# Kernel tuning notes

Hardware: AMD Instinct MI355X
Metric: run time of the kernel (lower is better)

Reference implementation:

```python
import jax, jax.numpy as jnp
import numpy as np

B, S, D, H = 2, 2048, 1024, 16
DK = D // H  # 64


def setup_inputs() -> dict:
    key = jax.random.key(0)
    k0, k1, k2, k3, k4, k5, k6 = jax.random.split(key, 7)
    scale = 0.02
    return {
        "q": jax.random.normal(k0, (B, S, D), dtype=jnp.float32),
        "k": jax.random.normal(k1, (B, S, D), dtype=jnp.float32),
        "v": jax.random.normal(k2, (B, S, D), dtype=jnp.float32),
        # per-head Q/K projection weights (n_head separate Linear layers, bias=False)
        "Wq": jax.random.normal(k3, (H, D, DK), dtype=jnp.float32) * scale,
        "Wk": jax.random.normal(k4, (H, D, DK), dtype=jnp.float32) * scale,
        # shared V projection (the same v_layer object is reused for every head)
        "Wv": jax.random.normal(k5, (D, DK), dtype=jnp.float32) * scale,
        # output projection fc: d_v -> d_model, bias=False
        "Wo": jax.random.normal(k6, (DK, D), dtype=jnp.float32) * scale,
    }


def reference(q, k, v, Wq, Wk, Wv, Wo):
    d_k = Wq.shape[-1]
    # batched per-head projections (replaces the Python loop over heads)
    qs = jnp.einsum("bsd,hdk->bhsk", q, Wq)          # [B,H,S,DK]
    ks = jnp.einsum("bsd,hdk->bhsk", k, Wk)          # [B,H,S,DK]
    vs = jnp.einsum("bsd,dk->bsk", v, Wv)            # [B,S,DK] shared across heads
    scores = jnp.einsum("bhsk,bhtk->bhst", qs, ks) / jnp.sqrt(
        jnp.asarray(d_k, dtype=jnp.float32)
    )                                                 # [B,H,S,S]
    attn = jax.nn.softmax(scores, axis=-1)            # [B,H,S,S]; dropout = identity (eval)
    heads = jnp.einsum("bhst,btk->bhsk", attn, vs)    # [B,H,S,DK]
    head = heads.mean(axis=1)                         # mean over heads, not concat
    attn_mean = attn.mean(axis=1)                     # [B,S,S]
    out = jnp.einsum("bsk,kd->bsd", head, Wo)         # [B,S,D]; dropout = identity
    return (out, attn_mean)
```

## Files before the change

### kernel.cpp

```cpp
#include <hip/hip_runtime.h>

#define B_ 2
#define S_ 2048
#define D_ 1024
#define H_ 16
#define DK_ 64

typedef __bf16 bf8 __attribute__((ext_vector_type(8)));
typedef float f4 __attribute__((ext_vector_type(4)));
typedef unsigned short u16x8 __attribute__((ext_vector_type(8)));

__device__ __forceinline__ unsigned short f2bf_bits(float f) {
  unsigned int u = __float_as_uint(f);
  return (unsigned short)((u + 0x7fffu + ((u >> 16) & 1u)) >> 16);
}

__device__ __forceinline__ bf8 pack_bf8(f4 lo, f4 hi) {
  u16x8 u;
  u[0] = f2bf_bits(lo[0]); u[1] = f2bf_bits(lo[1]);
  u[2] = f2bf_bits(lo[2]); u[3] = f2bf_bits(lo[3]);
  u[4] = f2bf_bits(hi[0]); u[5] = f2bf_bits(hi[1]);
  u[6] = f2bf_bits(hi[2]); u[7] = f2bf_bits(hi[3]);
  union { u16x8 u; bf8 b; } x; x.u = u; return x.b;
}

__device__ __forceinline__ bf8 ldb(const unsigned short* p) {
  return *reinterpret_cast<const bf8*>(p);
}

__device__ __forceinline__ void stage16(const void* g, void* l) {
  __builtin_amdgcn_global_load_lds(
      (const __attribute__((address_space(1))) void*)g,
      (__attribute__((address_space(3))) void*)l, 16, 0, 0);
}

#define MFMA(a, b, c) __builtin_amdgcn_mfma_f32_16x16x32_bf16((a), (b), (c), 0, 0, 0)

__global__ void k_prep(const float* __restrict__ q, const float* __restrict__ k,
                       const float* __restrict__ wq, const float* __restrict__ wk,
                       const float* __restrict__ wv, const float* __restrict__ wo,
                       unsigned short* __restrict__ qb, unsigned short* __restrict__ kb,
                       unsigned short* __restrict__ wqt, unsigned short* __restrict__ wkt,
                       unsigned short* __restrict__ wvt, unsigned short* __restrict__ wot) {
  __shared__ float tl[64 * 65];
  int bid = blockIdx.x, tid = threadIdx.x;
  const int rr = tid >> 6, cc = tid & 63;
  if (bid < 4096) {
    int which = bid >> 11;
    long i = ((long)(bid & 2047) * 256 + tid) * 8;
    const float* src = which ? k : q;
    unsigned short* dst = which ? kb : qb;
    f4 lo = *reinterpret_cast<const f4*>(src + i);
    f4 hi = *reinterpret_cast<const f4*>(src + i + 4);
    *reinterpret_cast<bf8*>(dst + i) = pack_bf8(lo, hi);
  } else if (bid < 4352) {
    int blk = bid - 4096;
    int h = blk >> 4, d0 = (blk & 15) * 64;
    for (int m = 0; m < 2; ++m) {
      const float* src = m ? wk : wq;
      unsigned short* dst = m ? wkt : wqt;
      if (m) __syncthreads();
#pragma unroll
      for (int it = 0; it < 16; ++it) {
        int d = it * 4 + rr;
        tl[cc * 65 + d] = src[(long)h * 65536 + (d0 + d) * 64 + cc];
      }
      __syncthreads();
#pragma unroll
      for (int it = 0; it < 16; ++it) {
        int n = it * 4 + rr;
        dst[(long)h * 65536 + n * 1024 + d0 + cc] = f2bf_bits(tl[n * 65 + cc]);
      }
    }
  } else if (bid < 4368) {
    int d0 = (bid - 4352) * 64;
#pragma unroll
    for (int it = 0; it < 16; ++it) {
      int d = it * 4 + rr;
      tl[cc * 65 + d] = wv[(long)(d0 + d) * 64 + cc];
    }
    __syncthreads();
#pragma unroll
    for (int it = 0; it < 16; ++it) {
      int n = it * 4 + rr;
      wvt[(long)n * 1024 + d0 + cc] = f2bf_bits(tl[n * 65 + cc]);
    }
  } else {
    int d0 = (bid - 4368) * 64;
#pragma unroll
    for (int it = 0; it < 16; ++it) {
      int kk = it * 4 + rr;
      tl[cc * 65 + kk] = wo[(long)kk * 1024 + d0 + cc];
    }
    __syncthreads();
#pragma unroll
    for (int it = 0; it < 16; ++it) {
      int ddl = it * 4 + rr;
      wot[(long)(d0 + ddl) * 64 + cc] = f2bf_bits(tl[ddl * 65 + cc]);
    }
  }
}

__global__ __launch_bounds__(256) void k_gemm_qk(
    const unsigned short* __restrict__ qb, const unsigned short* __restrict__ kb,
    const unsigned short* __restrict__ wqt, const unsigned short* __restrict__ wkt,
    unsigned short* __restrict__ qsb, unsigned short* __restrict__ ksb) {
  __shared__ unsigned short lds[8192];
  const int tid = threadIdx.x, wave = tid >> 6, lane = tid & 63;
  const int l15 = lane & 15, quad = lane >> 4;
  const int m0 = blockIdx.x * 128, n0 = blockIdx.y * 128;
  const int which = blockIdx.z;
  const unsigned short* A = which ? kb : qb;
  const unsigned short* W = which ? wkt : wqt;
  unsigned short* C = which ? ksb : qsb;
  const float scale = which ? 1.0f : 0.18033688011112042f;
  const int wr = wave >> 1, wc = wave & 1;

  f4 acc[4][4];
#pragma unroll
  for (int i = 0; i < 4; ++i)
#pragma unroll
    for (int j = 0; j < 4; ++j) acc[i][j] = f4{0.f, 0.f, 0.f, 0.f};

  const int sl15 = tid & 15, squad = (tid >> 4) & 3, st = tid >> 6;
  const unsigned short* gA = A + (long)(m0 + st * 16 + sl15) * D_ + squad * 8;
  const unsigned short* gB = W + (long)(n0 + st * 16 + sl15) * D_ + squad * 8;

  for (int k0 = 0; k0 < D_; k0 += 32) {
    stage16(gA + k0, lds + tid * 8);
    stage16(gA + 64 * D_ + k0, lds + 2048 + tid * 8);
    stage16(gB + k0, lds + 4096 + tid * 8);
    stage16(gB + 64 * D_ + k0, lds + 6144 + tid * 8);
    __syncthreads();
    bf8 aF[4], bF[4];
#pragma unroll
    for (int mi = 0; mi < 4; ++mi)
      aF[mi] = ldb(lds + (wr * 4 + mi) * 512 + lane * 8);
#pragma unroll
    for (int ni = 0; ni < 4; ++ni)
      bF[ni] = ldb(lds + 4096 + (wc * 4 + ni) * 512 + lane * 8);
#pragma unroll
    for (int mi = 0; mi < 4; ++mi)
#pragma unroll
      for (int ni = 0; ni < 4; ++ni)
        acc[mi][ni] = MFMA(aF[mi], bF[ni], acc[mi][ni]);
    __syncthreads();
  }
#pragma unroll
  for (int mi = 0; mi < 4; ++mi)
#pragma unroll
    for (int r = 0; r < 4; ++r) {
      long row = m0 + wr * 64 + mi * 16 + quad * 4 + r;
#pragma unroll
      for (int ni = 0; ni < 4; ++ni)
        C[row * D_ + n0 + wc * 64 + ni * 16 + l15] = f2bf_bits(acc[mi][ni][r] * scale);
    }
}

__global__ __launch_bounds__(256) void k_pv(
    const float* __restrict__ v, const unsigned short* __restrict__ wvt,
    float* __restrict__ pv) {
  const int tid = threadIdx.x, wave = tid >> 6, lane = tid & 63;
  const int l15 = lane & 15, quad = lane >> 4;
  const int rg = blockIdx.x, kc = blockIdx.y;
  const int row0 = rg * 64 + wave * 16;
  const float* arow = v + (long)(row0 + l15) * D_ + kc * 256 + quad * 8;
  const unsigned short* wbase = wvt + kc * 256 + quad * 8;
  f4 acc[4];
  for (int i = 0; i < 4; ++i) acc[i] = f4{0.f, 0.f, 0.f, 0.f};
  for (int k0 = 0; k0 < 256; k0 += 32) {
    f4 alo = *reinterpret_cast<const f4*>(arow + k0);
    f4 ahi = *reinterpret_cast<const f4*>(arow + k0 + 4);
    bf8 a = pack_bf8(alo, ahi);
#pragma unroll
    for (int i = 0; i < 4; ++i) {
      bf8 bf = ldb(wbase + (long)(i * 16 + l15) * D_ + k0);
      acc[i] = MFMA(a, bf, acc[i]);
    }
  }
#pragma unroll
  for (int i = 0; i < 4; ++i)
#pragma unroll
    for (int r = 0; r < 4; ++r)
      pv[((long)kc * 4096 + row0 + quad * 4 + r) * 64 + i * 16 + l15] = acc[i][r];
}

__global__ void k_vred(const float* __restrict__ pv, unsigned short* __restrict__ vst) {
  int e = blockIdx.x * 256 + threadIdx.x;
  int t = e & 2047, dk = (e >> 11) & 63, b = e >> 17;
  long row = (long)b * S_ + t;
  float s = pv[row * 64 + dk] + pv[(4096 + row) * 64 + dk] +
            pv[(8192 + row) * 64 + dk] + pv[(12288 + row) * 64 + dk];
  vst[e] = f2bf_bits(s);
}

__global__ __launch_bounds__(512) void k_denom(
    const unsigned short* __restrict__ qsb, const unsigned short* __restrict__ ksb,
    float* __restrict__ recip) {
  __shared__ unsigned short lds[16384];
  const int tid = threadIdx.x, wave = tid >> 6, lane = tid & 63;
  const int l15 = lane & 15, quad = lane >> 4;
  const int stile = blockIdx.x, h = blockIdx.y, b = blockIdx.z;
  const int s0 = stile * 128 + wave * 16;

  const unsigned short* qrow = qsb + ((long)(b * S_) + s0 + l15) * D_ + h * 64 + quad * 8;
  bf8 a0 = ldb(qrow);
  bf8 a1 = ldb(qrow + 32);

  const int sl15 = tid & 15, squad = (tid >> 4) & 3, stt = (tid >> 6) & 7;
  const unsigned short* g0 =
      ksb + ((long)(b * S_) + stt * 16 + sl15) * D_ + h * 64 + squad * 8;

  stage16(g0, lds + tid * 8);
  stage16(g0 + 32, lds + 4096 + tid * 8);
  asm volatile("s_waitcnt vmcnt(0)" ::: "memory");
  __builtin_amdgcn_s_barrier();
  int cur = 0;

  f4 sum = f4{0.f, 0.f, 0.f, 0.f};
  for (int it = 0; it < 16; ++it) {
    if (it + 1 < 16) {
      const unsigned short* gn = g0 + (long)(it + 1) * 128 * D_;
      unsigned short* nb = lds + (cur ^ 1) * 8192;
      stage16(gn, nb + tid * 8);
      stage16(gn + 32, nb + 4096 + tid * 8);
    }
    const unsigned short* base = lds + cur * 8192;
    __builtin_amdgcn_s_setprio(1);
#pragma unroll
    for (int tt = 0; tt < 8; ++tt) {
      bf8 b0 = ldb(base + tt * 512 + lane * 8);
      bf8 b1 = ldb(base + 4096 + tt * 512 + lane * 8);
      f4 d = f4{0.f, 0.f, 0.f, 0.f};
      d = MFMA(a0, b0, d);
      d = MFMA(a1, b1, d);
#pragma unroll
      for (int r = 0; r < 4; ++r) sum[r] += __builtin_amdgcn_exp2f(d[r]);
    }
    __builtin_amdgcn_s_setprio(0);
    if (it + 1 < 16) {
      asm volatile("s_waitcnt vmcnt(0)" ::: "memory");
      __builtin_amdgcn_s_barrier();
      cur ^= 1;
    }
  }
#pragma unroll
  for (int m = 1; m < 16; m <<= 1) {
#pragma unroll
    for (int r = 0; r < 4; ++r) sum[r] += __shfl_xor(sum[r], m, 64);
  }
  if (l15 == 0) {
    float* rp = recip + (long)(b * H_ + h) * S_ + s0 + quad * 4;
#pragma unroll
    for (int r = 0; r < 4; ++r) rp[r] = 1.0f / (16.0f * sum[r]);
  }
}

__global__ __launch_bounds__(512) void k_attn(
    const unsigned short* __restrict__ qsb, const unsigned short* __restrict__ ksb,
    const float* __restrict__ recip, float* __restrict__ am) {
  __shared__ unsigned short lds[16384];
  const int tid = threadIdx.x, wave = tid >> 6, lane = tid & 63;
  const int l15 = lane & 15, quad = lane >> 4;
  const int tchunk = blockIdx.x, stile = blockIdx.y, b = blockIdx.z;
  const int s0 = stile * 128 + wave * 16;
  const int t0c = tchunk * 128;

  f4 acc[8];
#pragma unroll
  for (int tt = 0; tt < 8; ++tt) acc[tt] = f4{0.f, 0.f, 0.f, 0.f};

  const unsigned short* qbase = qsb + ((long)(b * S_) + s0 + l15) * D_ + quad * 8;
  const int sl15 = tid & 15, squad = (tid >> 4) & 3, stt = (tid >> 6) & 7;
  const unsigned short* g0 =
      ksb + ((long)(b * S_) + t0c + stt * 16 + sl15) * D_ + squad * 8;
  const float* rbase = recip + (long)(b * H_) * S_ + s0 + quad * 4;

  stage16(g0, lds + tid * 8);
  stage16(g0 + 32, lds + 4096 + tid * 8);
  asm volatile("s_waitcnt vmcnt(0)" ::: "memory");
  __builtin_amdgcn_s_barrier();
  int cur = 0;

  for (int h = 0; h < H_; ++h) {
    if (h + 1 < H_) {
      const unsigned short* gn = g0 + (h + 1) * 64;
      unsigned short* nb = lds + (cur ^ 1) * 8192;
      stage16(gn, nb + tid * 8);
      stage16(gn + 32, nb + 4096 + tid * 8);
    }
    bf8 a0 = ldb(qbase + h * 64);
    bf8 a1 = ldb(qbase + h * 64 + 32);
    f4 rp = *reinterpret_cast<const f4*>(rbase + (long)h * S_);
    const unsigned short* base = lds + cur * 8192;
    __builtin_amdgcn_s_setprio(1);
#pragma unroll
    for (int tt = 0; tt < 8; ++tt) {
      bf8 b0 = ldb(base + tt * 512 + lane * 8);
      bf8 b1 = ldb(base + 4096 + tt * 512 + lane * 8);
      f4 d = f4{0.f, 0.f, 0.f, 0.f};
      d = MFMA(a0, b0, d);
      d = MFMA(a1, b1, d);
#pragma unroll
      for (int r = 0; r < 4; ++r) acc[tt][r] += rp[r] * __builtin_amdgcn_exp2f(d[r]);
    }
    __builtin_amdgcn_s_setprio(0);
    if (h + 1 < H_) {
      asm volatile("s_waitcnt vmcnt(0)" ::: "memory");
      __builtin_amdgcn_s_barrier();
      cur ^= 1;
    }
  }
  float* obase = am + ((long)b * S_ + s0 + quad * 4) * S_ + t0c + l15;
#pragma unroll
  for (int tt = 0; tt < 8; ++tt)
#pragma unroll
    for (int r = 0; r < 4; ++r) obase[(long)r * S_ + tt * 16] = acc[tt][r];
}

__global__ __launch_bounds__(256) void k_hpart(
    const float* __restrict__ am, const unsigned short* __restrict__ vst,
    float* __restrict__ ph) {
  const int tid = threadIdx.x, wave = tid >> 6, lane = tid & 63;
  const int l15 = lane & 15, quad = lane >> 4;
  const int rg = blockIdx.x, kc = blockIdx.y;
  const int row0 = rg * 64 + wave * 16;
  const int b = row0 >> 11;
  const float* arow = am + (long)(row0 + l15) * S_ + kc * 512 + quad * 8;
  const unsigned short* vb = vst + (long)b * DK_ * S_ + kc * 512 + quad * 8;
  f4 acc[4];
  for (int i = 0; i < 4; ++i) acc[i] = f4{0.f, 0.f, 0.f, 0.f};
  for (int t0 = 0; t0 < 512; t0 += 32) {
    f4 alo = *reinterpret_cast<const f4*>(arow + t0);
    f4 ahi = *reinterpret_cast<const f4*>(arow + t0 + 4);
    bf8 a = pack_bf8(alo, ahi);
#pragma unroll
    for (int i = 0; i < 4; ++i) {
      bf8 bf = ldb(vb + (long)(i * 16 + l15) * S_ + t0);
      acc[i] = MFMA(a, bf, acc[i]);
    }
  }
#pragma unroll
  for (int i = 0; i < 4; ++i)
#pragma unroll
    for (int r = 0; r < 4; ++r)
      ph[((long)kc * 4096 + row0 + quad * 4 + r) * 64 + i * 16 + l15] = acc[i][r];
}

__global__ void k_hred(const float* __restrict__ ph, unsigned short* __restrict__ headb) {
  int e = blockIdx.x * 256 + threadIdx.x;
  float s = ph[e] + ph[e + 4096 * 64] + ph[e + 2 * 4096 * 64] + ph[e + 3 * 4096 * 64];
  headb[e] = f2bf_bits(s);
}

__global__ __launch_bounds__(256) void k_out(
    const unsigned short* __restrict__ head, const unsigned short* __restrict__ wot,
    float* __restrict__ out) {
  const int tid = threadIdx.x, wave = tid >> 6, lane = tid & 63;
  const int l15 = lane & 15, quad = lane >> 4;
  const int dchunk = blockIdx.x, stile = blockIdx.y, b = blockIdx.z;
  const int s0 = stile * 64 + wave * 16;
  const int n0 = dchunk * 128;
  const unsigned short* hrow = head + ((long)b * S_ + s0 + l15) * DK_ + quad * 8;
  bf8 a0 = ldb(hrow);
  bf8 a1 = ldb(hrow + 32);
  const unsigned short* wb = wot + quad * 8;
  float* obase = out + ((long)b * S_ + s0 + quad * 4) * D_ + n0 + l15;
#pragma unroll
  for (int i = 0; i < 8; ++i) {
    const unsigned short* wp = wb + (long)(n0 + i * 16 + l15) * DK_;
    bf8 b0 = ldb(wp);
    bf8 b1 = ldb(wp + 32);
    f4 d = f4{0.f, 0.f, 0.f, 0.f};
    d = MFMA(a0, b0, d);
    d = MFMA(a1, b1, d);
#pragma unroll
    for (int r = 0; r < 4; ++r) obase[(long)r * D_ + i * 16] = d[r];
  }
}

extern "C" void kernel_launch(void* const* d_in, const int* in_sizes, int n_in,
                              void* d_out, int out_size, void* d_ws, size_t ws_size,
                              hipStream_t stream) {
  const float* q  = (const float*)d_in[0];
  const float* k  = (const float*)d_in[1];
  const float* v  = (const float*)d_in[2];
  const float* Wq = (const float*)d_in[3];
  const float* Wk = (const float*)d_in[4];
  const float* Wv = (const float*)d_in[5];
  const float* Wo = (const float*)d_in[6];

  float* out = (float*)d_out;
  float* am  = out + (long)B_ * S_ * D_;

  unsigned short* qsb  = (unsigned short*)d_ws;
  unsigned short* ksb  = qsb + 4194304;
  unsigned short* wqt  = ksb + 4194304;
  unsigned short* wkt  = wqt + 1048576;
  unsigned short* wvt  = wkt + 1048576;
  unsigned short* wot  = wvt + 65536;
  unsigned short* vst  = wot + 65536;
  unsigned short* headb= vst + 262144;
  float* recip = (float*)(headb + 262144);

  unsigned short* qb = (unsigned short*)am;
  unsigned short* kb = qb + 4194304;
  float* part = out;

  k_prep<<<4384, 256, 0, stream>>>(q, k, Wq, Wk, Wv, Wo, qb, kb, wqt, wkt, wvt, wot);
  k_gemm_qk<<<dim3(32, 8, 2), 256, 0, stream>>>(qb, kb, wqt, wkt, qsb, ksb);
  k_pv<<<dim3(64, 4), 256, 0, stream>>>(v, wvt, part);
  k_vred<<<1024, 256, 0, stream>>>(part, vst);
  k_denom<<<dim3(16, 16, 2), 512, 0, stream>>>(qsb, ksb, recip);
  k_attn<<<dim3(16, 16, 2), 512, 0, stream>>>(qsb, ksb, recip, am);
  k_hpart<<<dim3(64, 4), 256, 0, stream>>>(am, vst, part);
  k_hred<<<1024, 256, 0, stream>>>(part, headb);
  k_out<<<dim3(8, 32, 2), 256, 0, stream>>>(headb, wot, out);
}
```

Baseline: 243.5 us.

## Enlarge per-wave tiles in denom and attn kernels to reuse LDS K tiles

```diff
diff --git a/kernel.cpp b/kernel.cpp
--- a/kernel.cpp
+++ b/kernel.cpp
@@ -201,11 +201,13 @@
   const int tid = threadIdx.x, wave = tid >> 6, lane = tid & 63;
   const int l15 = lane & 15, quad = lane >> 4;
   const int stile = blockIdx.x, h = blockIdx.y, b = blockIdx.z;
-  const int s0 = stile * 128 + wave * 16;
+  const int s0 = stile * 256 + wave * 32;
 
   const unsigned short* qrow = qsb + ((long)(b * S_) + s0 + l15) * D_ + h * 64 + quad * 8;
   bf8 a0 = ldb(qrow);
   bf8 a1 = ldb(qrow + 32);
+  bf8 a2 = ldb(qrow + 16 * D_);
+  bf8 a3 = ldb(qrow + 16 * D_ + 32);
 
   const int sl15 = tid & 15, squad = (tid >> 4) & 3, stt = (tid >> 6) & 7;
   const unsigned short* g0 =
@@ -217,7 +219,7 @@
   __builtin_amdgcn_s_barrier();
   int cur = 0;
 
-  f4 sum = f4{0.f, 0.f, 0.f, 0.f};
+  f4 sum0 = f4{0.f, 0.f, 0.f, 0.f}, sum1 = f4{0.f, 0.f, 0.f, 0.f};
   for (int it = 0; it < 16; ++it) {
     if (it + 1 < 16) {
       const unsigned short* gn = g0 + (long)(it + 1) * 128 * D_;
@@ -234,8 +236,14 @@
       f4 d = f4{0.f, 0.f, 0.f, 0.f};
       d = MFMA(a0, b0, d);
       d = MFMA(a1, b1, d);
-#pragma unroll
-      for (int r = 0; r < 4; ++r) sum[r] += __builtin_amdgcn_exp2f(d[r]);
+      f4 e = f4{0.f, 0.f, 0.f, 0.f};
+      e = MFMA(a2, b0, e);
+      e = MFMA(a3, b1, e);
+#pragma unroll
+      for (int r = 0; r < 4; ++r) {
+        sum0[r] += __builtin_amdgcn_exp2f(d[r]);
+        sum1[r] += __builtin_amdgcn_exp2f(e[r]);
+      }
     }
     __builtin_amdgcn_s_setprio(0);
     if (it + 1 < 16) {
@@ -247,52 +255,70 @@
 #pragma unroll
   for (int m = 1; m < 16; m <<= 1) {
 #pragma unroll
-    for (int r = 0; r < 4; ++r) sum[r] += __shfl_xor(sum[r], m, 64);
+    for (int r = 0; r < 4; ++r) {
+      sum0[r] += __shfl_xor(sum0[r], m, 64);
+      sum1[r] += __shfl_xor(sum1[r], m, 64);
+    }
   }
   if (l15 == 0) {
     float* rp = recip + (long)(b * H_ + h) * S_ + s0 + quad * 4;
 #pragma unroll
-    for (int r = 0; r < 4; ++r) rp[r] = 1.0f / (16.0f * sum[r]);
+    for (int r = 0; r < 4; ++r) {
+      rp[r] = 1.0f / (16.0f * sum0[r]);
+      rp[r + 16] = 1.0f / (16.0f * sum1[r]);
+    }
   }
 }
 
 __global__ __launch_bounds__(512) void k_attn(
     const unsigned short* __restrict__ qsb, const unsigned short* __restrict__ ksb,
     const float* __restrict__ recip, float* __restrict__ am) {
-  __shared__ unsigned short lds[16384];
-  const int tid = threadIdx.x, wave = tid >> 6, lane = tid & 63;
-  const int l15 = lane & 15, quad = lane >> 4;
+  __shared__ unsigned short lds[32768];
+  const int tid = threadIdx.x, wave = tid >> 6, lane = tid & 63;
+  const int l15 = lane & 15, quad = lane >> 4;
+  const int ws = wave >> 1, wt = wave & 1;
   const int tchunk = blockIdx.x, stile = blockIdx.y, b = blockIdx.z;
-  const int s0 = stile * 128 + wave * 16;
-  const int t0c = tchunk * 128;
-
-  f4 acc[8];
-#pragma unroll
-  for (int tt = 0; tt < 8; ++tt) acc[tt] = f4{0.f, 0.f, 0.f, 0.f};
+  const int s0 = stile * 128 + ws * 32;
+  const int t0c = tchunk * 256;
+
+  f4 acc0[8], acc1[8];
+#pragma unroll
+  for (int tt = 0; tt < 8; ++tt) {
+    acc0[tt] = f4{0.f, 0.f, 0.f, 0.f};
+    acc1[tt] = f4{0.f, 0.f, 0.f, 0.f};
+  }
 
   const unsigned short* qbase = qsb + ((long)(b * S_) + s0 + l15) * D_ + quad * 8;
   const int sl15 = tid & 15, squad = (tid >> 4) & 3, stt = (tid >> 6) & 7;
-  const unsigned short* g0 =
+  const unsigned short* gsub0 =
       ksb + ((long)(b * S_) + t0c + stt * 16 + sl15) * D_ + squad * 8;
+  const unsigned short* gsub1 = gsub0 + 128 * D_;
   const float* rbase = recip + (long)(b * H_) * S_ + s0 + quad * 4;
 
-  stage16(g0, lds + tid * 8);
-  stage16(g0 + 32, lds + 4096 + tid * 8);
+  stage16(gsub0, lds + tid * 8);
+  stage16(gsub0 + 32, lds + 4096 + tid * 8);
+  stage16(gsub1, lds + 8192 + tid * 8);
+  stage16(gsub1 + 32, lds + 12288 + tid * 8);
   asm volatile("s_waitcnt vmcnt(0)" ::: "memory");
   __builtin_amdgcn_s_barrier();
   int cur = 0;
 
   for (int h = 0; h < H_; ++h) {
     if (h + 1 < H_) {
-      const unsigned short* gn = g0 + (h + 1) * 64;
-      unsigned short* nb = lds + (cur ^ 1) * 8192;
-      stage16(gn, nb + tid * 8);
-      stage16(gn + 32, nb + 4096 + tid * 8);
+      const int ho = (h + 1) * 64;
+      unsigned short* nb = lds + (cur ^ 1) * 16384;
+      stage16(gsub0 + ho, nb + tid * 8);
+      stage16(gsub0 + ho + 32, nb + 4096 + tid * 8);
+      stage16(gsub1 + ho, nb + 8192 + tid * 8);
+      stage16(gsub1 + ho + 32, nb + 12288 + tid * 8);
     }
     bf8 a0 = ldb(qbase + h * 64);
     bf8 a1 = ldb(qbase + h * 64 + 32);
-    f4 rp = *reinterpret_cast<const f4*>(rbase + (long)h * S_);
-    const unsigned short* base = lds + cur * 8192;
+    bf8 a2 = ldb(qbase + h * 64 + 16 * D_);
+    bf8 a3 = ldb(qbase + h * 64 + 16 * D_ + 32);
+    f4 rp0 = *reinterpret_cast<const f4*>(rbase + (long)h * S_);
+    f4 rp1 = *reinterpret_cast<const f4*>(rbase + (long)h * S_ + 16);
+    const unsigned short* base = lds + cur * 16384 + wt * 8192;
     __builtin_amdgcn_s_setprio(1);
 #pragma unroll
     for (int tt = 0; tt < 8; ++tt) {
@@ -301,8 +327,14 @@
       f4 d = f4{0.f, 0.f, 0.f, 0.f};
       d = MFMA(a0, b0, d);
       d = MFMA(a1, b1, d);
-#pragma unroll
-      for (int r = 0; r < 4; ++r) acc[tt][r] += rp[r] * __builtin_amdgcn_exp2f(d[r]);
+      f4 e = f4{0.f, 0.f, 0.f, 0.f};
+      e = MFMA(a2, b0, e);
+      e = MFMA(a3, b1, e);
+#pragma unroll
+      for (int r = 0; r < 4; ++r) {
+        acc0[tt][r] += rp0[r] * __builtin_amdgcn_exp2f(d[r]);
+        acc1[tt][r] += rp1[r] * __builtin_amdgcn_exp2f(e[r]);
+      }
     }
     __builtin_amdgcn_s_setprio(0);
     if (h + 1 < H_) {
@@ -311,11 +343,14 @@
       cur ^= 1;
     }
   }
-  float* obase = am + ((long)b * S_ + s0 + quad * 4) * S_ + t0c + l15;
+  float* obase = am + ((long)b * S_ + s0 + quad * 4) * S_ + t0c + wt * 128 + l15;
 #pragma unroll
   for (int tt = 0; tt < 8; ++tt)
 #pragma unroll
-    for (int r = 0; r < 4; ++r) obase[(long)r * S_ + tt * 16] = acc[tt][r];
+    for (int r = 0; r < 4; ++r) {
+      obase[(long)r * S_ + tt * 16] = acc0[tt][r];
+      obase[(long)(16 + r) * S_ + tt * 16] = acc1[tt][r];
+    }
 }
 
 __global__ __launch_bounds__(256) void k_hpart(
@@ -411,8 +446,8 @@
   k_gemm_qk<<<dim3(32, 8, 2), 256, 0, stream>>>(qb, kb, wqt, wkt, qsb, ksb);
   k_pv<<<dim3(64, 4), 256, 0, stream>>>(v, wvt, part);
   k_vred<<<1024, 256, 0, stream>>>(part, vst);
-  k_denom<<<dim3(16, 16, 2), 512, 0, stream>>>(qsb, ksb, recip);
-  k_attn<<<dim3(16, 16, 2), 512, 0, stream>>>(qsb, ksb, recip, am);
+  k_denom<<<dim3(8, 16, 2), 512, 0, stream>>>(qsb, ksb, recip);
+  k_attn<<<dim3(8, 16, 2), 512, 0, stream>>>(qsb, ksb, recip, am);
   k_hpart<<<dim3(64, 4), 256, 0, stream>>>(am, vst, part);
   k_hred<<<1024, 256, 0, stream>>>(part, headb);
   k_out<<<dim3(8, 32, 2), 256, 0, stream>>>(headb, wot, out);
```

Result: slower. 254.2 us (+4.4%).

## Switch denom and attention kernels to 32x32x16 MFMA tiles

Applied to the files above, without the earlier changes.

```diff
diff --git a/kernel.cpp b/kernel.cpp
--- a/kernel.cpp
+++ b/kernel.cpp
@@ -8,6 +8,7 @@
 
 typedef __bf16 bf8 __attribute__((ext_vector_type(8)));
 typedef float f4 __attribute__((ext_vector_type(4)));
+typedef float f16f __attribute__((ext_vector_type(16)));
 typedef unsigned short u16x8 __attribute__((ext_vector_type(8)));
 
 __device__ __forceinline__ unsigned short f2bf_bits(float f) {
@@ -35,6 +36,7 @@
 }
 
 #define MFMA(a, b, c) __builtin_amdgcn_mfma_f32_16x16x32_bf16((a), (b), (c), 0, 0, 0)
+#define MFMA32(a, b, c) __builtin_amdgcn_mfma_f32_32x32x16_bf16((a), (b), (c), 0, 0, 0)
 
 __global__ void k_prep(const float* __restrict__ q, const float* __restrict__ k,
                        const float* __restrict__ wq, const float* __restrict__ wk,
@@ -198,44 +200,51 @@
     const unsigned short* __restrict__ qsb, const unsigned short* __restrict__ ksb,
     float* __restrict__ recip) {
   __shared__ unsigned short lds[16384];
-  const int tid = threadIdx.x, wave = tid >> 6, lane = tid & 63;
-  const int l15 = lane & 15, quad = lane >> 4;
+  __shared__ float red[2][4][32];
+  const int tid = threadIdx.x, wave = tid >> 6, lane = tid & 63;
+  const int l31 = lane & 31, lh = lane >> 5;
+  const int ws = wave >> 1, wt = wave & 1;
   const int stile = blockIdx.x, h = blockIdx.y, b = blockIdx.z;
-  const int s0 = stile * 128 + wave * 16;
-
-  const unsigned short* qrow = qsb + ((long)(b * S_) + s0 + l15) * D_ + h * 64 + quad * 8;
-  bf8 a0 = ldb(qrow);
-  bf8 a1 = ldb(qrow + 32);
-
-  const int sl15 = tid & 15, squad = (tid >> 4) & 3, stt = (tid >> 6) & 7;
+  const int s0 = stile * 128 + ws * 32;
+
+  const unsigned short* qrow = qsb + ((long)(b * S_) + s0 + l31) * D_ + h * 64 + lh * 8;
+  bf8 aF[4];
+#pragma unroll
+  for (int k4 = 0; k4 < 4; ++k4) aF[k4] = ldb(qrow + k4 * 16);
+
+  const int t31s = tid & 31, khs = (tid >> 5) & 1, frs = (tid >> 6) & 7;
   const unsigned short* g0 =
-      ksb + ((long)(b * S_) + stt * 16 + sl15) * D_ + h * 64 + squad * 8;
+      ksb + ((long)(b * S_) + (frs >> 2) * 32 + t31s) * D_ + h * 64 + (frs & 3) * 16 + khs * 8;
 
   stage16(g0, lds + tid * 8);
-  stage16(g0 + 32, lds + 4096 + tid * 8);
+  stage16(g0 + 64 * D_, lds + 4096 + tid * 8);
   asm volatile("s_waitcnt vmcnt(0)" ::: "memory");
   __builtin_amdgcn_s_barrier();
   int cur = 0;
 
-  f4 sum = f4{0.f, 0.f, 0.f, 0.f};
+  f16f sum;
+#pragma unroll
+  for (int r = 0; r < 16; ++r) sum[r] = 0.f;
+
   for (int it = 0; it < 16; ++it) {
     if (it + 1 < 16) {
       const unsigned short* gn = g0 + (long)(it + 1) * 128 * D_;
       unsigned short* nb = lds + (cur ^ 1) * 8192;
       stage16(gn, nb + tid * 8);
-      stage16(gn + 32, nb + 4096 + tid * 8);
-    }
-    const unsigned short* base = lds + cur * 8192;
+      stage16(gn + 64 * D_, nb + 4096 + tid * 8);
+    }
+    const unsigned short* base = lds + cur * 8192 + wt * 4096;
     __builtin_amdgcn_s_setprio(1);
 #pragma unroll
-    for (int tt = 0; tt < 8; ++tt) {
-      bf8 b0 = ldb(base + tt * 512 + lane * 8);
-      bf8 b1 = ldb(base + 4096 + tt * 512 + lane * 8);
-      f4 d = f4{0.f, 0.f, 0.f, 0.f};
-      d = MFMA(a0, b0, d);
-      d = MFMA(a1, b1, d);
-#pragma unroll
-      for (int r = 0; r < 4; ++r) sum[r] += __builtin_amdgcn_exp2f(d[r]);
+    for (int t5 = 0; t5 < 2; ++t5) {
+      f16f d;
+#pragma unroll
+      for (int r = 0; r < 16; ++r) d[r] = 0.f;
+#pragma unroll
+      for (int k4 = 0; k4 < 4; ++k4)
+        d = MFMA32(aF[k4], ldb(base + t5 * 2048 + k4 * 512 + lane * 8), d);
+#pragma unroll
+      for (int r = 0; r < 16; ++r) sum[r] += __builtin_amdgcn_exp2f(d[r]);
     }
     __builtin_amdgcn_s_setprio(0);
     if (it + 1 < 16) {
@@ -245,14 +254,20 @@
     }
   }
 #pragma unroll
-  for (int m = 1; m < 16; m <<= 1) {
-#pragma unroll
-    for (int r = 0; r < 4; ++r) sum[r] += __shfl_xor(sum[r], m, 64);
-  }
-  if (l15 == 0) {
-    float* rp = recip + (long)(b * H_ + h) * S_ + s0 + quad * 4;
-#pragma unroll
-    for (int r = 0; r < 4; ++r) rp[r] = 1.0f / (16.0f * sum[r]);
+  for (int m = 1; m < 32; m <<= 1) {
+#pragma unroll
+    for (int r = 0; r < 16; ++r) sum[r] += __shfl_xor(sum[r], m, 64);
+  }
+  if (l31 == 0) {
+#pragma unroll
+    for (int r = 0; r < 16; ++r)
+      red[wt][ws][4 * lh + (r & 3) + 8 * (r >> 2)] = sum[r];
+  }
+  __syncthreads();
+  if (tid < 128) {
+    int wsi = tid >> 5, row = tid & 31;
+    float ssum = red[0][wsi][row] + red[1][wsi][row];
+    recip[(long)(b * H_ + h) * S_ + stile * 128 + wsi * 32 + row] = 1.0f / (16.0f * ssum);
   }
 }
 
@@ -261,48 +276,66 @@
     const float* __restrict__ recip, float* __restrict__ am) {
   __shared__ unsigned short lds[16384];
   const int tid = threadIdx.x, wave = tid >> 6, lane = tid & 63;
-  const int l15 = lane & 15, quad = lane >> 4;
+  const int l31 = lane & 31, lh = lane >> 5;
+  const int ws = wave >> 1, wt = wave & 1;
   const int tchunk = blockIdx.x, stile = blockIdx.y, b = blockIdx.z;
-  const int s0 = stile * 128 + wave * 16;
+  const int s0 = stile * 128 + ws * 32;
   const int t0c = tchunk * 128;
 
-  f4 acc[8];
-#pragma unroll
-  for (int tt = 0; tt < 8; ++tt) acc[tt] = f4{0.f, 0.f, 0.f, 0.f};
-
-  const unsigned short* qbase = qsb + ((long)(b * S_) + s0 + l15) * D_ + quad * 8;
-  const int sl15 = tid & 15, squad = (tid >> 4) & 3, stt = (tid >> 6) & 7;
-  const unsigned short* g0 =
-      ksb + ((long)(b * S_) + t0c + stt * 16 + sl15) * D_ + squad * 8;
-  const float* rbase = recip + (long)(b * H_) * S_ + s0 + quad * 4;
-
-  stage16(g0, lds + tid * 8);
-  stage16(g0 + 32, lds + 4096 + tid * 8);
+  f16f acc0, acc1;
+#pragma unroll
+  for (int r = 0; r < 16; ++r) { acc0[r] = 0.f; acc1[r] = 0.f; }
+
+  const unsigned short* qbase = qsb + ((long)(b * S_) + s0 + l31) * D_ + lh * 8;
+  const float* rbase = recip + (long)(b * H_) * S_ + s0 + 4 * lh;
+
+  const int t31s = tid & 31, khs = (tid >> 5) & 1, frs = (tid >> 6) & 7;
+  const unsigned short* ga =
+      ksb + ((long)(b * S_) + t0c + (frs >> 2) * 32 + t31s) * D_ + (frs & 3) * 16 + khs * 8;
+
+  stage16(ga, lds + tid * 8);
+  stage16(ga + 64 * D_, lds + 4096 + tid * 8);
   asm volatile("s_waitcnt vmcnt(0)" ::: "memory");
   __builtin_amdgcn_s_barrier();
   int cur = 0;
 
   for (int h = 0; h < H_; ++h) {
     if (h + 1 < H_) {
-      const unsigned short* gn = g0 + (h + 1) * 64;
+      const unsigned short* gn = ga + (h + 1) * 64;
       unsigned short* nb = lds + (cur ^ 1) * 8192;
       stage16(gn, nb + tid * 8);
-      stage16(gn + 32, nb + 4096 + tid * 8);
-    }
-    bf8 a0 = ldb(qbase + h * 64);
-    bf8 a1 = ldb(qbase + h * 64 + 32);
-    f4 rp = *reinterpret_cast<const f4*>(rbase + (long)h * S_);
-    const unsigned short* base = lds + cur * 8192;
+      stage16(gn + 64 * D_, nb + 4096 + tid * 8);
+    }
+    bf8 aF[4];
+#pragma unroll
+    for (int k4 = 0; k4 < 4; ++k4) aF[k4] = ldb(qbase + h * 64 + k4 * 16);
+    f4 rpq[4];
+#pragma unroll
+    for (int j = 0; j < 4; ++j)
+      rpq[j] = *reinterpret_cast<const f4*>(rbase + (long)h * S_ + j * 8);
+    const unsigned short* base = lds + cur * 8192 + wt * 4096;
     __builtin_amdgcn_s_setprio(1);
-#pragma unroll
-    for (int tt = 0; tt < 8; ++tt) {
-      bf8 b0 = ldb(base + tt * 512 + lane * 8);
-      bf8 b1 = ldb(base + 4096 + tt * 512 + lane * 8);
-      f4 d = f4{0.f, 0.f, 0.f, 0.f};
-      d = MFMA(a0, b0, d);
-      d = MFMA(a1, b1, d);
-#pragma unroll
-      for (int r = 0; r < 4; ++r) acc[tt][r] += rp[r] * __builtin_amdgcn_exp2f(d[r]);
+    {
+      f16f d;
+#pragma unroll
+      for (int r = 0; r < 16; ++r) d[r] = 0.f;
+#pragma unroll
+      for (int k4 = 0; k4 < 4; ++k4)
+        d = MFMA32(aF[k4], ldb(base + k4 * 512 + lane * 8), d);
+#pragma unroll
+      for (int r = 0; r < 16; ++r)
+        acc0[r] += rpq[r >> 2][r & 3] * __builtin_amdgcn_exp2f(d[r]);
+    }
+    {
+      f16f d;
+#pragma unroll
+      for (int r = 0; r < 16; ++r) d[r] = 0.f;
+#pragma unroll
+      for (int k4 = 0; k4 < 4; ++k4)
+        d = MFMA32(aF[k4], ldb(base + 2048 + k4 * 512 + lane * 8), d);
+#pragma unroll
+      for (int r = 0; r < 16; ++r)
+        acc1[r] += rpq[r >> 2][r & 3] * __builtin_amdgcn_exp2f(d[r]);
     }
     __builtin_amdgcn_s_setprio(0);
     if (h + 1 < H_) {
@@ -311,11 +344,13 @@
       cur ^= 1;
     }
   }
-  float* obase = am + ((long)b * S_ + s0 + quad * 4) * S_ + t0c + l15;
-#pragma unroll
-  for (int tt = 0; tt < 8; ++tt)
-#pragma unroll
-    for (int r = 0; r < 4; ++r) obase[(long)r * S_ + tt * 16] = acc[tt][r];
+  float* obase = am + ((long)b * S_ + s0 + 4 * lh) * S_ + t0c + wt * 64 + l31;
+#pragma unroll
+  for (int r = 0; r < 16; ++r) {
+    long ro = (long)((r & 3) + 8 * (r >> 2)) * S_;
+    obase[ro] = acc0[r];
+    obase[ro + 32] = acc1[r];
+  }
 }
 
 __global__ __launch_bounds__(256) void k_hpart(
```

After: 269.4 us. 1.11x slower.

## Retile denom and attn kernels to 32x64 wave tiles sharing K fragments

Applied to the files above, without the earlier changes.

```diff
diff --git a/kernel.cpp b/kernel.cpp
--- a/kernel.cpp
+++ b/kernel.cpp
@@ -198,14 +198,18 @@
     const unsigned short* __restrict__ qsb, const unsigned short* __restrict__ ksb,
     float* __restrict__ recip) {
   __shared__ unsigned short lds[16384];
-  const int tid = threadIdx.x, wave = tid >> 6, lane = tid & 63;
-  const int l15 = lane & 15, quad = lane >> 4;
+  __shared__ float red[2][4][32];
+  const int tid = threadIdx.x, wave = tid >> 6, lane = tid & 63;
+  const int l15 = lane & 15, quad = lane >> 4;
+  const int ws = wave >> 1, wt = wave & 1;
   const int stile = blockIdx.x, h = blockIdx.y, b = blockIdx.z;
-  const int s0 = stile * 128 + wave * 16;
+  const int s0 = stile * 128 + ws * 32;
 
   const unsigned short* qrow = qsb + ((long)(b * S_) + s0 + l15) * D_ + h * 64 + quad * 8;
   bf8 a0 = ldb(qrow);
   bf8 a1 = ldb(qrow + 32);
+  bf8 a2 = ldb(qrow + 16 * D_);
+  bf8 a3 = ldb(qrow + 16 * D_ + 32);
 
   const int sl15 = tid & 15, squad = (tid >> 4) & 3, stt = (tid >> 6) & 7;
   const unsigned short* g0 =
@@ -217,7 +221,7 @@
   __builtin_amdgcn_s_barrier();
   int cur = 0;
 
-  f4 sum = f4{0.f, 0.f, 0.f, 0.f};
+  f4 sum0 = f4{0.f, 0.f, 0.f, 0.f}, sum1 = f4{0.f, 0.f, 0.f, 0.f};
   for (int it = 0; it < 16; ++it) {
     if (it + 1 < 16) {
       const unsigned short* gn = g0 + (long)(it + 1) * 128 * D_;
@@ -225,17 +229,22 @@
       stage16(gn, nb + tid * 8);
       stage16(gn + 32, nb + 4096 + tid * 8);
     }
-    const unsigned short* base = lds + cur * 8192;
+    const unsigned short* base = lds + cur * 8192 + wt * 2048;
     __builtin_amdgcn_s_setprio(1);
 #pragma unroll
-    for (int tt = 0; tt < 8; ++tt) {
+    for (int tt = 0; tt < 4; ++tt) {
       bf8 b0 = ldb(base + tt * 512 + lane * 8);
       bf8 b1 = ldb(base + 4096 + tt * 512 + lane * 8);
-      f4 d = f4{0.f, 0.f, 0.f, 0.f};
-      d = MFMA(a0, b0, d);
-      d = MFMA(a1, b1, d);
-#pragma unroll
-      for (int r = 0; r < 4; ++r) sum[r] += __builtin_amdgcn_exp2f(d[r]);
+      f4 dA = f4{0.f, 0.f, 0.f, 0.f}, dB = f4{0.f, 0.f, 0.f, 0.f};
+      dA = MFMA(a0, b0, dA);
+      dB = MFMA(a2, b0, dB);
+      dA = MFMA(a1, b1, dA);
+      dB = MFMA(a3, b1, dB);
+#pragma unroll
+      for (int r = 0; r < 4; ++r) {
+        sum0[r] += __builtin_amdgcn_exp2f(dA[r]);
+        sum1[r] += __builtin_amdgcn_exp2f(dB[r]);
+      }
     }
     __builtin_amdgcn_s_setprio(0);
     if (it + 1 < 16) {
@@ -247,12 +256,23 @@
 #pragma unroll
   for (int m = 1; m < 16; m <<= 1) {
 #pragma unroll
-    for (int r = 0; r < 4; ++r) sum[r] += __shfl_xor(sum[r], m, 64);
+    for (int r = 0; r < 4; ++r) {
+      sum0[r] += __shfl_xor(sum0[r], m, 64);
+      sum1[r] += __shfl_xor(sum1[r], m, 64);
+    }
   }
   if (l15 == 0) {
-    float* rp = recip + (long)(b * H_ + h) * S_ + s0 + quad * 4;
-#pragma unroll
-    for (int r = 0; r < 4; ++r) rp[r] = 1.0f / (16.0f * sum[r]);
+#pragma unroll
+    for (int r = 0; r < 4; ++r) {
+      red[wt][ws][quad * 4 + r] = sum0[r];
+      red[wt][ws][16 + quad * 4 + r] = sum1[r];
+    }
+  }
+  __syncthreads();
+  if (tid < 128) {
+    int wsi = tid >> 5, row = tid & 31;
+    float ssum = red[0][wsi][row] + red[1][wsi][row];
+    recip[(long)(b * H_ + h) * S_ + stile * 128 + wsi * 32 + row] = 1.0f / (16.0f * ssum);
   }
 }
 
@@ -262,13 +282,17 @@
   __shared__ unsigned short lds[16384];
   const int tid = threadIdx.x, wave = tid >> 6, lane = tid & 63;
   const int l15 = lane & 15, quad = lane >> 4;
+  const int ws = wave >> 1, wt = wave & 1;
   const int tchunk = blockIdx.x, stile = blockIdx.y, b = blockIdx.z;
-  const int s0 = stile * 128 + wave * 16;
+  const int s0 = stile * 128 + ws * 32;
   const int t0c = tchunk * 128;
 
-  f4 acc[8];
-#pragma unroll
-  for (int tt = 0; tt < 8; ++tt) acc[tt] = f4{0.f, 0.f, 0.f, 0.f};
+  f4 acc0[4], acc1[4];
+#pragma unroll
+  for (int tt = 0; tt < 4; ++tt) {
+    acc0[tt] = f4{0.f, 0.f, 0.f, 0.f};
+    acc1[tt] = f4{0.f, 0.f, 0.f, 0.f};
+  }
 
   const unsigned short* qbase = qsb + ((long)(b * S_) + s0 + l15) * D_ + quad * 8;
   const int sl15 = tid & 15, squad = (tid >> 4) & 3, stt = (tid >> 6) & 7;
@@ -291,18 +315,26 @@
     }
     bf8 a0 = ldb(qbase + h * 64);
     bf8 a1 = ldb(qbase + h * 64 + 32);
-    f4 rp = *reinterpret_cast<const f4*>(rbase + (long)h * S_);
-    const unsigned short* base = lds + cur * 8192;
+    bf8 a2 = ldb(qbase + h * 64 + 16 * D_);
+    bf8 a3 = ldb(qbase + h * 64 + 16 * D_ + 32);
+    f4 rp0 = *reinterpret_cast<const f4*>(rbase + (long)h * S_);
+    f4 rp1 = *reinterpret_cast<const f4*>(rbase + (long)h * S_ + 16);
+    const unsigned short* base = lds + cur * 8192 + wt * 2048;
     __builtin_amdgcn_s_setprio(1);
 #pragma unroll
-    for (int tt = 0; tt < 8; ++tt) {
+    for (int tt = 0; tt < 4; ++tt) {
       bf8 b0 = ldb(base + tt * 512 + lane * 8);
       bf8 b1 = ldb(base + 4096 + tt * 512 + lane * 8);
-      f4 d = f4{0.f, 0.f, 0.f, 0.f};
-      d = MFMA(a0, b0, d);
-      d = MFMA(a1, b1, d);
-#pragma unroll
-      for (int r = 0; r < 4; ++r) acc[tt][r] += rp[r] * __builtin_amdgcn_exp2f(d[r]);
+      f4 dA = f4{0.f, 0.f, 0.f, 0.f}, dB = f4{0.f, 0.f, 0.f, 0.f};
+      dA = MFMA(a0, b0, dA);
+      dB = MFMA(a2, b0, dB);
+      dA = MFMA(a1, b1, dA);
+      dB = MFMA(a3, b1, dB);
+#pragma unroll
+      for (int r = 0; r < 4; ++r) {
+        acc0[tt][r] += rp0[r] * __builtin_amdgcn_exp2f(dA[r]);
+        acc1[tt][r] += rp1[r] * __builtin_amdgcn_exp2f(dB[r]);
+      }
     }
     __builtin_amdgcn_s_setprio(0);
     if (h + 1 < H_) {
@@ -311,11 +343,14 @@
       cur ^= 1;
     }
   }
-  float* obase = am + ((long)b * S_ + s0 + quad * 4) * S_ + t0c + l15;
-#pragma unroll
-  for (int tt = 0; tt < 8; ++tt)
-#pragma unroll
-    for (int r = 0; r < 4; ++r) obase[(long)r * S_ + tt * 16] = acc[tt][r];
+  float* obase = am + ((long)b * S_ + s0 + quad * 4) * S_ + t0c + wt * 64 + l15;
+#pragma unroll
+  for (int tt = 0; tt < 4; ++tt)
+#pragma unroll
+    for (int r = 0; r < 4; ++r) {
+      obase[(long)r * S_ + tt * 16] = acc0[tt][r];
+      obase[(long)(16 + r) * S_ + tt * 16] = acc1[tt][r];
+    }
 }
 
 __global__ __launch_bounds__(256) void k_hpart(
```

Measured after the change: 260.0 us. 1.07x slower.
